# Kernel optimization log

Measured on AMD Instinct MI355X. Metric: run time of the kernel, lower is better.

## Reference

```python
import jax, jax.numpy as jnp
import numpy as np

D_MODEL = 1024
N_EXPERTS = 4
TOP_K = 32


def setup_inputs() -> dict:
    key = jax.random.key(0)
    k1, k2, k3, k4 = jax.random.split(key, 4)
    b, t, d = 2, 2048, D_MODEL
    n_lts = 8192
    h = jax.random.normal(k1, (b, t, d), dtype=jnp.float32)
    lts = jax.random.normal(k2, (1, n_lts, d), dtype=jnp.float32)
    # router: nn.Linear(d_model, n_experts)
    lim = 1.0 / np.sqrt(d)
    W_router = jax.random.uniform(k3, (N_EXPERTS, d), minval=-lim, maxval=lim, dtype=jnp.float32)
    b_router = jax.random.uniform(k4, (N_EXPERTS,), minval=-lim, maxval=lim, dtype=jnp.float32)
    return {"h": h, "lts": lts, "W_router": W_router, "b_router": b_router}


def reference(h, lts, W_router, b_router):
    b, t, d = h.shape
    n_lts = lts.shape[1]
    top_k = TOP_K
    n_experts = N_EXPERTS

    # router (eval mode: no noise)
    logits = jnp.einsum('btd,ed->bte', h, W_router) + b_router  # (b,t,E)
    expert_weights = jax.nn.softmax(logits, axis=-1)
    expert_idx = jnp.argmax(expert_weights, axis=-1)            # (b,t) int

    entries_per_expert = n_lts // n_experts
    offsets = jnp.minimum(expert_idx * entries_per_expert, n_lts - top_k)  # (b,t)
    indices = offsets[..., None] + jnp.arange(top_k)            # (b,t,k)
    indices = jnp.minimum(indices, n_lts - 1)

    # gather memory slices: lts broadcast over batch -> (b,t,k,d)
    selected = jnp.take(lts[0], indices, axis=0)

    # small attention of each token over its top_k memory entries
    scores = jnp.einsum('btd,btkd->btk', h, selected) / jnp.sqrt(jnp.asarray(d, h.dtype))
    attn = jax.nn.softmax(scores, axis=-1)
    result = jnp.einsum('btk,btkd->btd', attn, selected)
    return result, expert_weights
```

## Files before the change

### kernel.cpp

```cpp
#include <hip/hip_runtime.h>
#include <hip/hip_fp16.h>
#include <math.h>

constexpr int D    = 1024;
constexpr int NEXP = 4;
constexpr int EPP  = 2048;

typedef _Float16 f16x8 __attribute__((ext_vector_type(8)));
typedef float    f32x4 __attribute__((ext_vector_type(4)));

__device__ __forceinline__ unsigned pk2(float a, float b) {
    return __builtin_bit_cast(unsigned, __builtin_amdgcn_cvt_pkrtz(a, b));
}

__global__ __launch_bounds__(256) void prep_kernel(
    const float* __restrict__ lts, _Float16* __restrict__ lts16,
    _Float16* __restrict__ ltsT)
{
    const int e = blockIdx.x >> 4, part = (blockIdx.x >> 2) & 3, dc = blockIdx.x & 3;
    const int tid = threadIdx.x;
    __shared__ __align__(16) _Float16 s[8][256];

    const float4* src = reinterpret_cast<const float4*>(lts);
    #pragma unroll
    for (int i = 0; i < 2; ++i) {
        const int f = tid + 256 * i;
        const int r = f >> 6, c4 = f & 63;
        const float4 v = src[(size_t)(e * EPP + part * 8 + r) * 256 + dc * 64 + c4];
        *reinterpret_cast<uint2*>(&s[r][c4 * 4]) = make_uint2(pk2(v.x, v.y), pk2(v.z, v.w));
    }
    __syncthreads();

    {
        const int r = tid >> 5, c = tid & 31;
        *reinterpret_cast<uint4*>(lts16 + (size_t)(e * 32 + part * 8 + r) * D + dc * 256 + c * 8) =
            *reinterpret_cast<const uint4*>(&s[r][c * 8]);
    }
    {
        _Float16 tmp[8];
        #pragma unroll
        for (int k = 0; k < 8; ++k) tmp[k] = s[k][tid];
        *reinterpret_cast<uint4*>(ltsT + ((size_t)e << 15) + (size_t)(dc * 256 + tid) * 32 + part * 8) =
            *reinterpret_cast<const uint4*>(tmp);
    }
}

__global__ __launch_bounds__(256) void qk_kernel(
    const float* __restrict__ h, const _Float16* __restrict__ lts16,
    const float* __restrict__ Wr, const float* __restrict__ br,
    float* __restrict__ out_ew, _Float16* __restrict__ P32,
    int* __restrict__ eidx, int ntok)
{
    const int tid = threadIdx.x, wid = tid >> 6, lane = tid & 63;
    const int base = blockIdx.x * 8;

    __shared__ __align__(16) unsigned char h_lds[8 * 2048];
    __shared__ int experts[8];

    {
        const int r = tid >> 5, c = tid & 31;
        int tok = base + r; if (tok > ntok - 1) tok = ntok - 1;
        const float4* src = reinterpret_cast<const float4*>(h + (size_t)tok * D);
        #pragma unroll
        for (int i = 0; i < 4; ++i) {
            const int g = c + 32 * i;
            const float4 a = src[2 * g];
            const float4 b = src[2 * g + 1];
            uint4 u;
            u.x = pk2(a.x, a.y); u.y = pk2(a.z, a.w);
            u.z = pk2(b.x, b.y); u.w = pk2(b.z, b.w);
            *reinterpret_cast<uint4*>(h_lds + r * 2048 + ((g ^ r) << 4)) = u;
        }
    }

    {
        const float4* h4 = reinterpret_cast<const float4*>(h);
        const float4* w4 = reinterpret_cast<const float4*>(Wr);
        float4 wf[NEXP][4];
        #pragma unroll
        for (int e = 0; e < NEXP; ++e)
            #pragma unroll
            for (int i = 0; i < 4; ++i)
                wf[e][i] = w4[e * 256 + lane + 64 * i];
        const float bb0 = br[0], bb1 = br[1], bb2 = br[2], bb3 = br[3];

        #pragma unroll
        for (int t = 0; t < 2; ++t) {
            const int tok = base + wid * 2 + t;
            if (tok < ntok) {
                float acc[NEXP] = {0.f, 0.f, 0.f, 0.f};
                #pragma unroll
                for (int i = 0; i < 4; ++i) {
                    const float4 a = h4[(size_t)tok * 256 + lane + 64 * i];
                    #pragma unroll
                    for (int e = 0; e < NEXP; ++e)
                        acc[e] += a.x * wf[e][i].x + a.y * wf[e][i].y
                                + a.z * wf[e][i].z + a.w * wf[e][i].w;
                }
                #pragma unroll
                for (int m = 1; m < 64; m <<= 1)
                    #pragma unroll
                    for (int e = 0; e < NEXP; ++e) acc[e] += __shfl_xor(acc[e], m);
                const float l0 = acc[0] + bb0, l1 = acc[1] + bb1,
                            l2 = acc[2] + bb2, l3 = acc[3] + bb3;
                const float lm = fmaxf(fmaxf(l0, l1), fmaxf(l2, l3));
                const float e0 = __expf(l0 - lm), e1 = __expf(l1 - lm),
                            e2 = __expf(l2 - lm), e3 = __expf(l3 - lm);
                const float einv = 1.f / (e0 + e1 + e2 + e3);
                if (lane < NEXP) {
                    const float ev = (lane == 0) ? e0 : (lane == 1) ? e1 : (lane == 2) ? e2 : e3;
                    out_ew[(size_t)tok * NEXP + lane] = ev * einv;
                }
                int bi = 0; float bv = l0;
                if (l1 > bv) { bv = l1; bi = 1; }
                if (l2 > bv) { bv = l2; bi = 2; }
                if (l3 > bv) { bv = l3; bi = 3; }
                if (lane == 0) experts[wid * 2 + t] = bi;
            } else if (lane == 0) experts[wid * 2 + t] = 0;
        }
    }
    __syncthreads();

    const int rA = lane & 15, g4 = lane >> 4, arow = rA & 7;

    f32x4 s0 = {0.f, 0.f, 0.f, 0.f}, s1 = {0.f, 0.f, 0.f, 0.f};
    const _Float16* b0p = lts16 + (size_t)(wid * 32 + rA) * D + g4 * 8;
    const _Float16* b1p = b0p + 16 * D;
    #pragma unroll
    for (int kc = 0; kc < 32; ++kc) {
        const f16x8 a = *reinterpret_cast<const f16x8*>(
            h_lds + arow * 2048 + ((((kc << 2) | g4) ^ arow) << 4));
        const f16x8 b0 = *reinterpret_cast<const f16x8*>(b0p + kc * 32);
        const f16x8 b1 = *reinterpret_cast<const f16x8*>(b1p + kc * 32);
        s0 = __builtin_amdgcn_mfma_f32_16x16x32_f16(a, b0, s0, 0, 0, 0);
        s1 = __builtin_amdgcn_mfma_f32_16x16x32_f16(a, b1, s1, 0, 0, 0);
    }

    constexpr float inv32 = 1.f / 32.f;
    #pragma unroll
    for (int r = 0; r < 4; ++r) {
        const int tr = g4 * 4 + r;
        if (tr < 8 && base + tr < ntok && experts[tr] == wid) {
            float mx = fmaxf(s0[r], s1[r]);
            #pragma unroll
            for (int m = 1; m < 16; m <<= 1) mx = fmaxf(mx, __shfl_xor(mx, m));
            const float e0 = __expf((s0[r] - mx) * inv32);
            const float e1 = __expf((s1[r] - mx) * inv32);
            float sm = e0 + e1;
            #pragma unroll
            for (int m = 1; m < 16; m <<= 1) sm += __shfl_xor(sm, m);
            const float is = 1.f / sm;
            const int tok2 = base + tr;
            P32[(size_t)tok2 * 32 + rA]      = (_Float16)(e0 * is);
            P32[(size_t)tok2 * 32 + rA + 16] = (_Float16)(e1 * is);
            if (rA == 0) eidx[tok2] = wid;
        }
    }
}

__global__ __launch_bounds__(256) void pv_kernel(
    const _Float16* __restrict__ P32, const int* __restrict__ eidx,
    const _Float16* __restrict__ ltsT, float* __restrict__ out_res, int ntok)
{
    const int tile = blockIdx.x >> 2, q = blockIdx.x & 3;
    const int tid = threadIdx.x, wid = tid >> 6, lane = tid & 63;
    __shared__ __align__(16) unsigned char p_lds[16 * 256];

    {
        const int r = tid >> 4, c = tid & 15;
        const int tok = tile * 16 + r;
        uint4 v = make_uint4(0, 0, 0, 0);
        if (tok < ntok) {
            const int ex = eidx[tok];
            if ((c >> 2) == ex)
                v = *reinterpret_cast<const uint4*>(P32 + (size_t)tok * 32 + (c & 3) * 8);
        }
        *reinterpret_cast<uint4*>(p_lds + r * 256 + ((c ^ (r & 7)) << 4)) = v;
    }
    __syncthreads();

    const int rA = lane & 15, g4 = lane >> 4;
    f16x8 pa[4];
    #pragma unroll
    for (int kc = 0; kc < 4; ++kc)
        pa[kc] = *reinterpret_cast<const f16x8*>(
            p_lds + rA * 256 + ((((kc << 2) | g4) ^ (rA & 7)) << 4));

    int toks[4];
    #pragma unroll
    for (int r = 0; r < 4; ++r) toks[r] = tile * 16 + g4 * 4 + r;

    #pragma unroll
    for (int i = 0; i < 4; ++i) {
        const int dimc = q * 256 + wid * 64 + i * 16 + rA;
        f32x4 o = {0.f, 0.f, 0.f, 0.f};
        #pragma unroll
        for (int kc = 0; kc < 4; ++kc) {
            const f16x8 bk = *reinterpret_cast<const f16x8*>(
                ltsT + ((size_t)kc << 15) + (size_t)dimc * 32 + g4 * 8);
            o = __builtin_amdgcn_mfma_f32_16x16x32_f16(pa[kc], bk, o, 0, 0, 0);
        }
        #pragma unroll
        for (int r = 0; r < 4; ++r)
            if (toks[r] < ntok) out_res[(size_t)toks[r] * D + dimc] = o[r];
    }
}

extern "C" void kernel_launch(void* const* d_in, const int* in_sizes, int n_in,
                              void* d_out, int out_size, void* d_ws, size_t ws_size,
                              hipStream_t stream) {
    const float* h   = (const float*)d_in[0];
    const float* lts = (const float*)d_in[1];
    const float* Wr  = (const float*)d_in[2];
    const float* br  = (const float*)d_in[3];

    const int ntok = in_sizes[0] / D;
    float* out_res = (float*)d_out;
    float* out_ew  = out_res + (size_t)ntok * D;

    _Float16* lts16 = (_Float16*)d_ws;
    _Float16* ltsT  = lts16 + (size_t)128 * D;
    _Float16* P32   = ltsT + (size_t)NEXP * D * 32;
    int*      eidx  = (int*)(P32 + (size_t)ntok * 32);

    prep_kernel<<<64, 256, 0, stream>>>(lts, lts16, ltsT);
    qk_kernel<<<(ntok + 7) / 8, 256, 0, stream>>>(h, lts16, Wr, br, out_ew, P32, eidx, ntok);
    pv_kernel<<<((ntok + 15) / 16) * 4, 256, 0, stream>>>(P32, eidx, ltsT, out_res, ntok);
}
```

Before: 39.86 us.

## Split router into its own kernel and parallelize QK over experts with split-K

Moves the router softmax/argmax and the fp16 conversion of h into a separate kernel that writes h16 and expert indices to workspace. The QK kernel then launches one block per (expert, 16-token chunk), with the four waves splitting the K dimension and reducing partial scores through LDS. This gives the QK step more blocks in flight and removes the per-block serial router work. In exchange it adds a kernel launch, writes and re-reads an fp16 copy of h through global memory, and computes QK for all four experts per token even though only one is kept.

```diff
diff --git a/kernel.cpp b/kernel.cpp
--- a/kernel.cpp
+++ b/kernel.cpp
@@ -45,116 +45,118 @@
     }
 }
 
+__global__ __launch_bounds__(256) void router_kernel(
+    const float* __restrict__ h, const float* __restrict__ Wr,
+    const float* __restrict__ br, float* __restrict__ out_ew,
+    int* __restrict__ eidx, _Float16* __restrict__ h16, int ntok)
+{
+    const int tid = threadIdx.x, wid = tid >> 6, lane = tid & 63;
+    const int tok = blockIdx.x * 4 + wid;
+    if (tok >= ntok) return;
+
+    const float4* h4 = reinterpret_cast<const float4*>(h);
+    const float4* w4 = reinterpret_cast<const float4*>(Wr);
+
+    float4 av[4];
+    float acc[NEXP] = {0.f, 0.f, 0.f, 0.f};
+    #pragma unroll
+    for (int i = 0; i < 4; ++i) {
+        av[i] = h4[(size_t)tok * 256 + lane + 64 * i];
+        #pragma unroll
+        for (int e = 0; e < NEXP; ++e) {
+            const float4 w = w4[e * 256 + lane + 64 * i];
+            acc[e] += av[i].x * w.x + av[i].y * w.y + av[i].z * w.z + av[i].w * w.w;
+        }
+    }
+    #pragma unroll
+    for (int m = 1; m < 64; m <<= 1)
+        #pragma unroll
+        for (int e = 0; e < NEXP; ++e) acc[e] += __shfl_xor(acc[e], m);
+
+    const float l0 = acc[0] + br[0], l1 = acc[1] + br[1],
+                l2 = acc[2] + br[2], l3 = acc[3] + br[3];
+    const float lm = fmaxf(fmaxf(l0, l1), fmaxf(l2, l3));
+    const float e0 = __expf(l0 - lm), e1 = __expf(l1 - lm),
+                e2 = __expf(l2 - lm), e3 = __expf(l3 - lm);
+    const float einv = 1.f / (e0 + e1 + e2 + e3);
+    if (lane < NEXP) {
+        const float ev = (lane == 0) ? e0 : (lane == 1) ? e1 : (lane == 2) ? e2 : e3;
+        out_ew[(size_t)tok * NEXP + lane] = ev * einv;
+    }
+    int bi = 0; float bv = l0;
+    if (l1 > bv) { bv = l1; bi = 1; }
+    if (l2 > bv) { bv = l2; bi = 2; }
+    if (l3 > bv) { bv = l3; bi = 3; }
+    if (lane == 0) eidx[tok] = bi;
+
+    #pragma unroll
+    for (int i = 0; i < 4; ++i)
+        *reinterpret_cast<uint2*>(h16 + (size_t)tok * D + (lane + 64 * i) * 4) =
+            make_uint2(pk2(av[i].x, av[i].y), pk2(av[i].z, av[i].w));
+}
+
 __global__ __launch_bounds__(256) void qk_kernel(
-    const float* __restrict__ h, const _Float16* __restrict__ lts16,
-    const float* __restrict__ Wr, const float* __restrict__ br,
-    float* __restrict__ out_ew, _Float16* __restrict__ P32,
-    int* __restrict__ eidx, int ntok)
-{
+    const _Float16* __restrict__ h16, const _Float16* __restrict__ lts16,
+    const int* __restrict__ eidx, _Float16* __restrict__ P32,
+    int ntok, int chunks)
+{
+    const int e = blockIdx.x / chunks;
+    const int chunk = blockIdx.x - e * chunks;
+    const int base = chunk * 16;
+
     const int tid = threadIdx.x, wid = tid >> 6, lane = tid & 63;
-    const int base = blockIdx.x * 8;
-
-    __shared__ __align__(16) unsigned char h_lds[8 * 2048];
-    __shared__ int experts[8];
-
-    {
-        const int r = tid >> 5, c = tid & 31;
-        int tok = base + r; if (tok > ntok - 1) tok = ntok - 1;
-        const float4* src = reinterpret_cast<const float4*>(h + (size_t)tok * D);
-        #pragma unroll
-        for (int i = 0; i < 4; ++i) {
-            const int g = c + 32 * i;
-            const float4 a = src[2 * g];
-            const float4 b = src[2 * g + 1];
-            uint4 u;
-            u.x = pk2(a.x, a.y); u.y = pk2(a.z, a.w);
-            u.z = pk2(b.x, b.y); u.w = pk2(b.z, b.w);
-            *reinterpret_cast<uint4*>(h_lds + r * 2048 + ((g ^ r) << 4)) = u;
-        }
-    }
-
-    {
-        const float4* h4 = reinterpret_cast<const float4*>(h);
-        const float4* w4 = reinterpret_cast<const float4*>(Wr);
-        float4 wf[NEXP][4];
-        #pragma unroll
-        for (int e = 0; e < NEXP; ++e)
-            #pragma unroll
-            for (int i = 0; i < 4; ++i)
-                wf[e][i] = w4[e * 256 + lane + 64 * i];
-        const float bb0 = br[0], bb1 = br[1], bb2 = br[2], bb3 = br[3];
-
-        #pragma unroll
-        for (int t = 0; t < 2; ++t) {
-            const int tok = base + wid * 2 + t;
-            if (tok < ntok) {
-                float acc[NEXP] = {0.f, 0.f, 0.f, 0.f};
-                #pragma unroll
-                for (int i = 0; i < 4; ++i) {
-                    const float4 a = h4[(size_t)tok * 256 + lane + 64 * i];
-                    #pragma unroll
-                    for (int e = 0; e < NEXP; ++e)
-                        acc[e] += a.x * wf[e][i].x + a.y * wf[e][i].y
-                                + a.z * wf[e][i].z + a.w * wf[e][i].w;
-                }
-                #pragma unroll
-                for (int m = 1; m < 64; m <<= 1)
-                    #pragma unroll
-                    for (int e = 0; e < NEXP; ++e) acc[e] += __shfl_xor(acc[e], m);
-                const float l0 = acc[0] + bb0, l1 = acc[1] + bb1,
-                            l2 = acc[2] + bb2, l3 = acc[3] + bb3;
-                const float lm = fmaxf(fmaxf(l0, l1), fmaxf(l2, l3));
-                const float e0 = __expf(l0 - lm), e1 = __expf(l1 - lm),
-                            e2 = __expf(l2 - lm), e3 = __expf(l3 - lm);
-                const float einv = 1.f / (e0 + e1 + e2 + e3);
-                if (lane < NEXP) {
-                    const float ev = (lane == 0) ? e0 : (lane == 1) ? e1 : (lane == 2) ? e2 : e3;
-                    out_ew[(size_t)tok * NEXP + lane] = ev * einv;
-                }
-                int bi = 0; float bv = l0;
-                if (l1 > bv) { bv = l1; bi = 1; }
-                if (l2 > bv) { bv = l2; bi = 2; }
-                if (l3 > bv) { bv = l3; bi = 3; }
-                if (lane == 0) experts[wid * 2 + t] = bi;
-            } else if (lane == 0) experts[wid * 2 + t] = 0;
-        }
-    }
-    __syncthreads();
-
-    const int rA = lane & 15, g4 = lane >> 4, arow = rA & 7;
+    __shared__ int eix[16];
+    __shared__ float S_part[4][16][33];
+
+    if (tid < 16) {
+        const int tk = base + tid;
+        eix[tid] = (tk < ntok) ? eidx[tk] : -1;
+    }
+    __syncthreads();
+
+    const int rA = lane & 15, g4 = lane >> 4;
+    int hr = base + rA; if (hr > ntok - 1) hr = ntok - 1;
+    const _Float16* ap  = h16  + (size_t)hr * D + g4 * 8;
+    const _Float16* b0p = lts16 + (size_t)(e * 32 + rA) * D + g4 * 8;
+    const _Float16* b1p = b0p + 16 * D;
 
     f32x4 s0 = {0.f, 0.f, 0.f, 0.f}, s1 = {0.f, 0.f, 0.f, 0.f};
-    const _Float16* b0p = lts16 + (size_t)(wid * 32 + rA) * D + g4 * 8;
-    const _Float16* b1p = b0p + 16 * D;
-    #pragma unroll
-    for (int kc = 0; kc < 32; ++kc) {
-        const f16x8 a = *reinterpret_cast<const f16x8*>(
-            h_lds + arow * 2048 + ((((kc << 2) | g4) ^ arow) << 4));
+    #pragma unroll
+    for (int k = 0; k < 8; ++k) {
+        const int kc = wid * 8 + k;
+        const f16x8 a  = *reinterpret_cast<const f16x8*>(ap + kc * 32);
         const f16x8 b0 = *reinterpret_cast<const f16x8*>(b0p + kc * 32);
         const f16x8 b1 = *reinterpret_cast<const f16x8*>(b1p + kc * 32);
         s0 = __builtin_amdgcn_mfma_f32_16x16x32_f16(a, b0, s0, 0, 0, 0);
         s1 = __builtin_amdgcn_mfma_f32_16x16x32_f16(a, b1, s1, 0, 0, 0);
     }
-
+    #pragma unroll
+    for (int r = 0; r < 4; ++r) {
+        S_part[wid][g4 * 4 + r][rA]      = s0[r];
+        S_part[wid][g4 * 4 + r][rA + 16] = s1[r];
+    }
+    __syncthreads();
+
+    const int tr = tid >> 4, sl = tid & 15;
+    const float v0 = S_part[0][tr][sl] + S_part[1][tr][sl]
+                   + S_part[2][tr][sl] + S_part[3][tr][sl];
+    const float v1 = S_part[0][tr][sl + 16] + S_part[1][tr][sl + 16]
+                   + S_part[2][tr][sl + 16] + S_part[3][tr][sl + 16];
     constexpr float inv32 = 1.f / 32.f;
-    #pragma unroll
-    for (int r = 0; r < 4; ++r) {
-        const int tr = g4 * 4 + r;
-        if (tr < 8 && base + tr < ntok && experts[tr] == wid) {
-            float mx = fmaxf(s0[r], s1[r]);
-            #pragma unroll
-            for (int m = 1; m < 16; m <<= 1) mx = fmaxf(mx, __shfl_xor(mx, m));
-            const float e0 = __expf((s0[r] - mx) * inv32);
-            const float e1 = __expf((s1[r] - mx) * inv32);
-            float sm = e0 + e1;
-            #pragma unroll
-            for (int m = 1; m < 16; m <<= 1) sm += __shfl_xor(sm, m);
-            const float is = 1.f / sm;
-            const int tok2 = base + tr;
-            P32[(size_t)tok2 * 32 + rA]      = (_Float16)(e0 * is);
-            P32[(size_t)tok2 * 32 + rA + 16] = (_Float16)(e1 * is);
-            if (rA == 0) eidx[tok2] = wid;
-        }
+    float mx = fmaxf(v0, v1);
+    #pragma unroll
+    for (int m = 1; m < 16; m <<= 1) mx = fmaxf(mx, __shfl_xor(mx, m));
+    const float p0 = __expf((v0 - mx) * inv32);
+    const float p1 = __expf((v1 - mx) * inv32);
+    float sm = p0 + p1;
+    #pragma unroll
+    for (int m = 1; m < 16; m <<= 1) sm += __shfl_xor(sm, m);
+    const float is = 1.f / sm;
+
+    const int tok = base + tr;
+    if (tok < ntok && eix[tr] == e) {
+        P32[(size_t)tok * 32 + sl]      = (_Float16)(p0 * is);
+        P32[(size_t)tok * 32 + sl + 16] = (_Float16)(p1 * is);
     }
 }
 
@@ -222,8 +224,12 @@
     _Float16* ltsT  = lts16 + (size_t)128 * D;
     _Float16* P32   = ltsT + (size_t)NEXP * D * 32;
     int*      eidx  = (int*)(P32 + (size_t)ntok * 32);
+    _Float16* h16   = (_Float16*)(eidx + ntok);
+
+    const int chunks = (ntok + 15) / 16;
 
     prep_kernel<<<64, 256, 0, stream>>>(lts, lts16, ltsT);
-    qk_kernel<<<(ntok + 7) / 8, 256, 0, stream>>>(h, lts16, Wr, br, out_ew, P32, eidx, ntok);
-    pv_kernel<<<((ntok + 15) / 16) * 4, 256, 0, stream>>>(P32, eidx, ltsT, out_res, ntok);
-}
+    router_kernel<<<(ntok + 3) / 4, 256, 0, stream>>>(h, Wr, br, out_ew, eidx, h16, ntok);
+    qk_kernel<<<NEXP * chunks, 256, 0, stream>>>(h16, lts16, eidx, P32, ntok, chunks);
+    pv_kernel<<<chunks * 4, 256, 0, stream>>>(P32, eidx, ltsT, out_res, ntok);
+}
```

After: 39.88 us. About the same (+0.1%).
